# Kernel tuning notes

Hardware: AMD Instinct MI355X
Metric: run time of the kernel (lower is better)

The kernel has to match this reference:

```python
import jax, jax.numpy as jnp
import numpy as np

# Model constants (from module __init__ / repo script)
DT = 60                    # model time step [s]
DT_FORCING = 3600          # forcing time step [s]
NSUB = DT_FORCING // DT    # substeps between forcing samples = 60
NT = 5_040_000             # number of model steps (~9.6 years at dt=60s)
NF = NT // NSUB            # forcing series length = 84000
FC = 1e-4                  # Coriolis frequency


def setup_inputs() -> dict:
    key = jax.random.key(0)
    k1, k2, k3 = jax.random.split(key, 3)
    # pk = log(K); K ~ exp(-10) ~ 4.5e-5 keeps the Euler recurrence stable (|a|<1)
    pk = -10.0 + 0.1 * jax.random.normal(k1, (2,), dtype=jnp.float32)
    # wind stress forcing, around the repo's 0.2 N/m^2 zonal value
    TAx = 0.2 + 0.05 * jax.random.normal(k2, (NF,), dtype=jnp.float32)
    TAy = 0.05 * jax.random.normal(k3, (NF,), dtype=jnp.float32)
    return {"pk": pk, "TAx": TAx, "TAy": TAy}


def reference(pk, TAx, TAy):
    K = jnp.exp(pk)                                    # K[0]: wind coeff, K[1]: damping
    TA = TAx.astype(jnp.complex64) + 1j * TAy.astype(jnp.complex64)  # [NF]

    # Vectorized linear interpolation of forcing onto every model step it=0..NT-2
    it = jnp.arange(NT - 1)
    itf = it // NSUB
    aa = (it % NSUB).astype(jnp.float32) / NSUB
    # faithful to original: compares against NT (never true), then relies on
    # JAX's clamping gather for the final out-of-range itf+1
    itsup = jnp.where(itf + 1 >= NT, -1, itf + 1)
    TAi = (1.0 - aa) * TA[itf] + aa * TA[itsup]        # [NT-1] complex64

    # U_{t+1} = U_t + dt*(-i*fc*U_t + K0*TA_t - K1*U_t) = a*U_t + b_t
    a = jnp.asarray(1.0 + DT * (-1j * FC - K[1]), dtype=jnp.complex64)
    b = (DT * K[0]).astype(jnp.complex64) * TAi        # [NT-1]

    def step(u, bt):
        u_next = a * u + bt
        return u_next, u_next

    u0 = jnp.zeros((), dtype=jnp.complex64)
    _, ys = jax.lax.scan(step, u0, b)                  # [NT-1]
    U = jnp.concatenate([u0[None], ys])                # [NT], U[0] = 0
    return jnp.real(U), jnp.imag(U)
```

## Files before the change

### kernel.cpp

```cpp
#include <hip/hip_runtime.h>
#include <math.h>

#define NTOT   5040000
#define NFORC  84000
#define NSUB_  60
#define NSTEPS (NTOT - 1)

#define TPB     256
#define SEGS    60
#define WIN     (TPB * SEGS)
#define WARM    4800
#define CHUNK   (WIN - WARM)
#define TILE    30
#define TSTRIDE 31

__global__ __launch_bounds__(TPB, 2)
void slab_scan_kernel(const float* __restrict__ pk,
                      const float* __restrict__ TAx,
                      const float* __restrict__ TAy,
                      float* __restrict__ out)
{
    __shared__ float2 tb[TPB * TSTRIDE];

    const int tid = threadIdx.x;
    const int blk = blockIdx.x;

    const float K0 = expf(pk[0]);
    const float K1 = expf(pk[1]);
    const float ar = 1.0f - 60.0f * K1;
    const float ai = -60.0f * 1.0e-4f;
    const float s  = 60.0f * K0;

    const int wstart = blk * CHUNK;
    const int wend   = min(wstart + CHUNK, NSTEPS);
    const int ws     = max(0, wstart - WARM);

    const int itf = ws / NSUB_ + tid;
    const int i0  = min(itf,     NFORC - 1);
    const int i1  = min(itf + 1, NFORC - 1);
    const float x0 = TAx[i0], y0 = TAy[i0];
    const float x1 = TAx[i1], y1 = TAy[i1];
    const float cinv = s * (1.0f / 60.0f);
    const float dxs  = (x1 - x0) * cinv;
    const float dys  = (y1 - y0) * cinv;
    const float b0re = s * x0;
    const float b0im = s * y0;

    float ur = 0.f, ui = 0.f;
    {
        float bre = b0re, bim = b0im;
        #pragma unroll
        for (int k = 0; k < SEGS; ++k) {
            float nr = fmaf(ar, ur, fmaf(-ai, ui, bre));
            float ni = fmaf(ar, ui, fmaf( ai, ur, bim));
            ur = nr; ui = ni;
            bre += dxs; bim += dys;
        }
    }

    float2 apow[8];
    {
        double br_ = (double)ar, bi_ = (double)ai;
        double prr = 1.0, pii = 0.0;
        int e = SEGS;
        while (e) {
            if (e & 1) { double t = prr*br_ - pii*bi_; pii = prr*bi_ + pii*br_; prr = t; }
            double t = br_*br_ - bi_*bi_; bi_ = 2.0*br_*bi_; br_ = t;
            e >>= 1;
        }
        double cr = prr, ci = pii;
        #pragma unroll
        for (int k = 0; k < 8; ++k) {
            apow[k] = make_float2((float)cr, (float)ci);
            double t = cr*cr - ci*ci; ci = 2.0*cr*ci; cr = t;
        }
    }

    float2 v = make_float2(ur, ui);
    tb[tid] = v;
    __syncthreads();
    #pragma unroll
    for (int k = 0; k < 8; ++k) {
        const int off = 1 << k;
        float2 prev = make_float2(0.f, 0.f);
        if (tid >= off) prev = tb[tid - off];
        __syncthreads();
        v.x = fmaf(apow[k].x, prev.x, fmaf(-apow[k].y, prev.y, v.x));
        v.y = fmaf(apow[k].x, prev.y, fmaf( apow[k].y, prev.x, v.y));
        tb[tid] = v;
        __syncthreads();
    }
    float usr = 0.f, usi = 0.f;
    if (tid > 0) { float2 p = tb[tid - 1]; usr = p.x; usi = p.y; }
    __syncthreads();

    ur = usr; ui = usi;
    float bre = b0re, bim = b0im;
    for (int h = 0; h < SEGS / TILE; ++h) {
        #pragma unroll
        for (int k = 0; k < TILE; ++k) {
            float nr = fmaf(ar, ur, fmaf(-ai, ui, bre));
            float ni = fmaf(ar, ui, fmaf( ai, ur, bim));
            ur = nr; ui = ni;
            bre += dxs; bim += dys;
            tb[tid * TSTRIDE + k] = make_float2(nr, ni);
        }
        __syncthreads();
        {
            int row = tid / TILE;
            int k   = tid - row * TILE;
            for (int i = 0; i < TILE; ++i) {
                float2 w = tb[row * TSTRIDE + k];
                const int o = ws + row * SEGS + h * TILE + k;
                if (o >= wstart && o < wend) {
                    out[o + 1]        = w.x;
                    out[NTOT + o + 1] = w.y;
                }
                row += 8; k += 16;
                if (k >= TILE) { k -= TILE; row += 1; }
            }
        }
        __syncthreads();
    }

    if (blk == 0 && tid == 0) { out[0] = 0.f; out[NTOT] = 0.f; }
}

extern "C" void kernel_launch(void* const* d_in, const int* in_sizes, int n_in,
                              void* d_out, int out_size, void* d_ws, size_t ws_size,
                              hipStream_t stream)
{
    const float* pk  = (const float*)d_in[0];
    const float* TAx = (const float*)d_in[1];
    const float* TAy = (const float*)d_in[2];
    float* out = (float*)d_out;

    const int nblocks = (NSTEPS + CHUNK - 1) / CHUNK;
    slab_scan_kernel<<<dim3(nblocks), dim3(TPB), 0, stream>>>(pk, TAx, TAy, out);
}
```

Baseline: 78.59 us.

## Use wavefront shuffle scan, smaller XOR-swizzled tile, and higher occupancy

Replaces the 8-level shared-memory block scan with a 6-level wavefront shuffle scan plus a small cross-wave combine, removing most block-wide barriers. The output staging tile shrinks from 30 to 15 steps with an XOR swizzle instead of padding, which cuts LDS use so launch bounds can request 5 blocks per CU instead of 2. Threads whose segment lies entirely in the warm-up region skip the recompute pass. The cost is more tile iterations and barriers in the write phase, plus some extra per-lane complex-power arithmetic.

```diff
diff --git a/kernel.cpp b/kernel.cpp
--- a/kernel.cpp
+++ b/kernel.cpp
@@ -11,19 +11,27 @@
 #define WIN     (TPB * SEGS)
 #define WARM    4800
 #define CHUNK   (WIN - WARM)
-#define TILE    30
-#define TSTRIDE 31
+#define TILE    15
+#define NTILES  (SEGS / TILE)
+#define TSTR    (TILE + 1)
 
-__global__ __launch_bounds__(TPB, 2)
+__device__ __forceinline__ float2 cmadd(float2 a, float2 p, float2 c) {
+    return make_float2(fmaf(a.x, p.x, fmaf(-a.y, p.y, c.x)),
+                       fmaf(a.x, p.y, fmaf( a.y, p.x, c.y)));
+}
+
+__global__ __launch_bounds__(TPB, 5)
 void slab_scan_kernel(const float* __restrict__ pk,
                       const float* __restrict__ TAx,
                       const float* __restrict__ TAy,
                       float* __restrict__ out)
 {
-    __shared__ float2 tb[TPB * TSTRIDE];
+    __shared__ float2 tb[TPB * TSTR];
 
-    const int tid = threadIdx.x;
-    const int blk = blockIdx.x;
+    const int tid  = threadIdx.x;
+    const int lane = tid & 63;
+    const int wv   = tid >> 6;
+    const int blk  = blockIdx.x;
 
     const float K0 = expf(pk[0]);
     const float K1 = expf(pk[1]);
@@ -58,7 +66,7 @@
         }
     }
 
-    float2 apow[8];
+    float2 apow[7];
     {
         double br_ = (double)ar, bi_ = (double)ai;
         double prr = 1.0, pii = 0.0;
@@ -70,54 +78,80 @@
         }
         double cr = prr, ci = pii;
         #pragma unroll
-        for (int k = 0; k < 8; ++k) {
+        for (int k = 0; k < 7; ++k) {
             apow[k] = make_float2((float)cr, (float)ci);
             double t = cr*cr - ci*ci; ci = 2.0*cr*ci; cr = t;
         }
     }
 
     float2 v = make_float2(ur, ui);
-    tb[tid] = v;
+    #pragma unroll
+    for (int k = 0; k < 6; ++k) {
+        const int off = 1 << k;
+        float px = __shfl_up(v.x, off);
+        float py = __shfl_up(v.y, off);
+        if (lane >= off) v = cmadd(apow[k], make_float2(px, py), v);
+    }
+    float ex = __shfl_up(v.x, 1);
+    float ey = __shfl_up(v.y, 1);
+    float2 E = (lane == 0) ? make_float2(0.f, 0.f) : make_float2(ex, ey);
+
+    if (lane == 63) tb[wv] = v;
     __syncthreads();
-    #pragma unroll
-    for (int k = 0; k < 8; ++k) {
-        const int off = 1 << k;
-        float2 prev = make_float2(0.f, 0.f);
-        if (tid >= off) prev = tb[tid - off];
-        __syncthreads();
-        v.x = fmaf(apow[k].x, prev.x, fmaf(-apow[k].y, prev.y, v.x));
-        v.y = fmaf(apow[k].x, prev.y, fmaf( apow[k].y, prev.x, v.y));
-        tb[tid] = v;
-        __syncthreads();
+    float2 P = make_float2(0.f, 0.f);
+    {
+        float2 t0 = tb[0], t1 = tb[1], t2 = tb[2];
+        if (wv >= 1) P = t0;
+        if (wv >= 2) P = cmadd(apow[6], P, t1);
+        if (wv >= 3) P = cmadd(apow[6], P, t2);
     }
-    float usr = 0.f, usi = 0.f;
-    if (tid > 0) { float2 p = tb[tid - 1]; usr = p.x; usi = p.y; }
     __syncthreads();
 
-    ur = usr; ui = usi;
+    float2 aL = make_float2(1.f, 0.f);
+    #pragma unroll
+    for (int k = 0; k < 6; ++k) {
+        if ((lane >> k) & 1) {
+            aL = make_float2(aL.x*apow[k].x - aL.y*apow[k].y,
+                             aL.x*apow[k].y + aL.y*apow[k].x);
+        }
+    }
+    const float2 us = cmadd(aL, P, E);
+
+    const int  seg_lo = ws + tid * SEGS;
+    const bool live   = (seg_lo + (SEGS - 1) >= wstart) && (seg_lo < wend);
+    const int  sx     = tid & 15;
+
+    float pur = us.x, pui = us.y;
     float bre = b0re, bim = b0im;
-    for (int h = 0; h < SEGS / TILE; ++h) {
-        #pragma unroll
-        for (int k = 0; k < TILE; ++k) {
-            float nr = fmaf(ar, ur, fmaf(-ai, ui, bre));
-            float ni = fmaf(ar, ui, fmaf( ai, ur, bim));
-            ur = nr; ui = ni;
-            bre += dxs; bim += dys;
-            tb[tid * TSTRIDE + k] = make_float2(nr, ni);
+
+    int row0 = tid / TILE;
+    int k0   = tid - row0 * TILE;
+
+    for (int h = 0; h < NTILES; ++h) {
+        if (live) {
+            #pragma unroll
+            for (int k = 0; k < TILE; ++k) {
+                float nr = fmaf(ar, pur, fmaf(-ai, pui, bre));
+                float ni = fmaf(ar, pui, fmaf( ai, pur, bim));
+                pur = nr; pui = ni;
+                bre += dxs; bim += dys;
+                tb[(tid << 4) + (k ^ sx)] = make_float2(nr, ni);
+            }
         }
         __syncthreads();
         {
-            int row = tid / TILE;
-            int k   = tid - row * TILE;
+            int row = row0, kk = k0;
+            const int base = ws + h * TILE;
+            #pragma unroll
             for (int i = 0; i < TILE; ++i) {
-                float2 w = tb[row * TSTRIDE + k];
-                const int o = ws + row * SEGS + h * TILE + k;
+                float2 w = tb[(row << 4) + (kk ^ (row & 15))];
+                const int o = base + row * SEGS + kk;
                 if (o >= wstart && o < wend) {
                     out[o + 1]        = w.x;
                     out[NTOT + o + 1] = w.y;
                 }
-                row += 8; k += 16;
-                if (k >= TILE) { k -= TILE; row += 1; }
+                row += 17; kk += 1;
+                if (kk >= TILE) { kk -= TILE; row += 1; }
             }
         }
         __syncthreads();
```

New measurement: 80.34 us. 1.02x slower.
